# Performance work log

Hardware: AMD Instinct MI355X
Metric: run time of the kernel (lower is better)

The kernel has to match this reference:

```python
import jax, jax.numpy as jnp
import numpy as np
from jax import lax

NH = 8        # num_heads
C = 256       # embedding_dim
WS = 5        # window_size
DN = ('NCHW', 'OIHW', 'NCHW')


def setup_inputs() -> dict:
    key = jax.random.key(0)
    ks = jax.random.split(key, 6)
    B, H, W = 16, 64, 64
    hd = C // NH  # per-head dim = pos_embed_dim
    return {
        "src": jax.random.normal(ks[0], (B, C, H, W), jnp.float32),
        "rel_pos_embed": jax.random.normal(ks[1], (hd, WS, WS), jnp.float32) * 0.02,
        "qkv_w": jax.random.normal(ks[2], (3 * C, C), jnp.float32) * (C ** -0.5),
        "cpe_w": jax.random.normal(ks[3], (C, C, 3, 3), jnp.float32) * (1.0 / np.sqrt(C * 9)),
        "cpe_b": jnp.zeros((C,), jnp.float32),
        "out_w": jax.random.normal(ks[4], (C, C), jnp.float32) * (C ** -0.5),
        "out_b": jnp.zeros((C,), jnp.float32),
    }


def reference(src, rel_pos_embed, qkv_w, cpe_w, cpe_b, out_w, out_b):
    B, Cc, H, W = src.shape
    hd = Cc // NH
    scale = hd ** -0.5

    # conv positional encoding (3x3 conv) + residual
    x = lax.conv_general_dilated(src, cpe_w, (1, 1), [(1, 1), (1, 1)],
                                 dimension_numbers=DN) + cpe_b[None, :, None, None] + src

    # 1x1 qkv conv as a GEMM over channels
    qkv = jnp.einsum('oc,bchw->bohw', qkv_w, x)
    q, k, v = jnp.split(qkv, 3, axis=1)
    q = q.reshape(B * NH, hd, H, W)
    k = k.reshape(B * NH, hd, H, W)
    v = v.reshape(B * NH, hd, H, W)

    # linear (lambda) attention: softmax over spatial positions of k
    kf = jax.nn.softmax(k.reshape(B * NH, hd, H * W), axis=-1)   # (b' i n)
    vf = v.reshape(B * NH, hd, H * W)                            # (b' o n)
    content_lambda = jnp.einsum('bin,bon->bio', kf, vf)          # (b' i o), tiny
    qf = q.reshape(B * NH, hd, H * W) * scale
    content = jnp.einsum('bin,bio->bon', qf, content_lambda).reshape(B * NH, hd, H, W)

    # depthwise conv positional lambda on v
    pad = WS // 2
    pos_lambda = lax.conv_general_dilated(v, rel_pos_embed[:, None], (1, 1),
                                          [(pad, pad), (pad, pad)],
                                          dimension_numbers=DN,
                                          feature_group_count=hd)
    result = (content + q * pos_lambda).reshape(B, Cc, H, W)

    # 1x1 output projection
    return jnp.einsum('oc,bchw->bohw', out_w, result) + out_b[None, :, None, None]
```

## Files before the change

kernel.cpp:

```cpp
#include <hip/hip_runtime.h>


typedef unsigned short u16;
typedef __bf16 bf16x8 __attribute__((ext_vector_type(8)));
typedef float f32x4 __attribute__((ext_vector_type(4)));
#define HW 4096

__device__ __forceinline__ float bf2f(u16 u){
  unsigned v = ((unsigned)u) << 16;
  return __builtin_bit_cast(float, v);
}
__device__ __forceinline__ u16 f2bf(float f){
  unsigned u = __builtin_bit_cast(unsigned, f);
  u = u + 0x7fffu + ((u >> 16) & 1u);
  return (u16)(u >> 16);
}
__device__ __forceinline__ unsigned pack2(float a, float b){
  return (unsigned)f2bf(a) | ((unsigned)f2bf(b) << 16);
}
__device__ __forceinline__ void unpack2(unsigned u, float& a, float& b){
  a = bf2f((u16)(u & 0xffffu)); b = bf2f((u16)(u >> 16));
}
__device__ __forceinline__ void unp8(uint4 r, float* v){
  unpack2(r.x, v[0], v[1]); unpack2(r.y, v[2], v[3]);
  unpack2(r.z, v[4], v[5]); unpack2(r.w, v[6], v[7]);
}
__device__ __forceinline__ int swz(int p){ return (p&3) ^ ((p>>2)&3); }

__device__ __forceinline__ void gl2lds16(const u16* g, u16* l){
  __builtin_amdgcn_global_load_lds((__attribute__((address_space(1))) void*)g,
                                   (__attribute__((address_space(3))) void*)l, 16, 0, 0);
}

__global__ void zero_border(u16* __restrict__ xpad){
  int idx = blockIdx.x*256 + threadIdx.x;
  int g = idx & 31;
  int p = idx >> 5;
  int b = p / 260; int r = p - b*260;
  int y, x;
  if (r < 66)      { y = 0;      x = r; }
  else if (r < 132){ y = 65;     x = r-66; }
  else if (r < 196){ y = r-131;  x = 0; }
  else             { y = r-195;  x = 65; }
  *(uint4*)&xpad[((size_t)b*4356 + (size_t)y*66 + x)*256 + g*8] = uint4{0,0,0,0};
}

__global__ __launch_bounds__(256) void to_nhwc(const float* __restrict__ src,
                                               u16* __restrict__ xpad){
  __shared__ u16 sl[64*264];
  const int t = threadIdx.x, w = t>>6, lane = t&63;
  const int y = blockIdx.x, b = blockIdx.y;
  for (int cc = 0; cc < 64; ++cc){
    const int c = cc*4 + w;
    float v = src[((size_t)(b*256 + c))*HW + y*64 + lane];
    sl[lane*264 + c] = f2bf(v);
  }
  __syncthreads();
  #pragma unroll
  for (int i = 0; i < 8; ++i){
    int idx = t + 256*i;
    int p = idx >> 5, g = idx & 31;
    uint4 v = *(const uint4*)&sl[p*264 + g*8];
    *(uint4*)&xpad[((size_t)b*4356 + (size_t)(y+1)*66 + (p+1))*256 + g*8] = v;
  }
}

__global__ void repack_w(const float* __restrict__ cpe_w, const float* __restrict__ qkv_w,
                         const float* __restrict__ out_w, u16* __restrict__ wrb,
                         u16* __restrict__ wq, u16* __restrict__ wo){
  int idx = blockIdx.x*256 + threadIdx.x;
  if (idx < 589824){
    int kk = idx >> 16, o = (idx >> 8) & 255, c = idx & 255;
    wrb[idx] = f2bf(cpe_w[((o*256 + c)*9) + kk]);
  } else if (idx < 786432){
    int j = idx - 589824;
    wq[j] = f2bf(qkv_w[j]);
  } else {
    int j = idx - 786432;
    wo[j] = f2bf(out_w[j]);
  }
}

__global__ __launch_bounds__(256) void conv_mfma(const u16* __restrict__ xpad,
    const u16* __restrict__ wrb, const float* __restrict__ bias,
    u16* __restrict__ xout){
  __shared__ u16 As[4096];
  __shared__ u16 Bs[4096];
  const int t = threadIdx.x, w = t>>6, lane = t&63;
  const int idx = blockIdx.x;
  const int x8 = idx&7, q = idx>>3;
  const int ot = q & 1, nb = (q>>1)*8 + x8;
  const int pg = nb*128;
  const int b = pg>>12, hw0 = pg&4095, y0 = hw0>>6;
  const int o0 = ot*128;
  const size_t xb = (size_t)b*4356;
  const int sp = t>>2;
  const int cs = (t&3) ^ swz(sp);
  const u16* agp0 = xpad + (xb + (size_t)(y0+1)*66 + sp + 1)*256 + cs*8;
  const u16* agp1 = agp0 + 66*256;
  const u16* bgp0 = wrb + (size_t)(o0 + sp)*256 + cs*8;
  const u16* bgp1 = bgp0 + 64*256;
  const int wm = w&1, wn = w>>1;
  int a_off[4], b_off[4];
  #pragma unroll
  for (int i = 0; i < 4; ++i){
    int p = wm*64 + i*16 + (lane&15);
    a_off[i] = p*32 + ((((lane>>4) ^ swz(p)) & 3) << 3);
    int r = wn*64 + i*16 + (lane&15);
    b_off[i] = r*32 + ((((lane>>4) ^ swz(r)) & 3) << 3);
  }
  f32x4 acc[4][4];
  #pragma unroll
  for (int i=0;i<4;++i)
    #pragma unroll
    for (int j=0;j<4;++j) acc[i][j] = f32x4{0.f,0.f,0.f,0.f};

  for (int c0 = 0; c0 < 256; c0 += 32){
    for (int kk = 0; kk < 9; ++kk){
      const int toff = ((kk/3 - 1)*66 + (kk%3 - 1))*256;
      __syncthreads();
      gl2lds16(agp0 + toff + c0, &As[t*8]);
      gl2lds16(agp1 + toff + c0, &As[2048 + t*8]);
      gl2lds16(bgp0 + kk*65536 + c0, &Bs[t*8]);
      gl2lds16(bgp1 + kk*65536 + c0, &Bs[2048 + t*8]);
      __syncthreads();
      bf16x8 af[4], bfr[4];
      #pragma unroll
      for (int i = 0; i < 4; ++i){
        af[i]  = __builtin_bit_cast(bf16x8, *(const uint4*)&As[a_off[i]]);
        bfr[i] = __builtin_bit_cast(bf16x8, *(const uint4*)&Bs[b_off[i]]);
      }
      #pragma unroll
      for (int mt = 0; mt < 4; ++mt)
        #pragma unroll
        for (int nt = 0; nt < 4; ++nt)
          acc[mt][nt] = __builtin_amdgcn_mfma_f32_16x16x32_bf16(bfr[nt], af[mt], acc[mt][nt], 0,0,0);
    }
  }
  #pragma unroll
  for (int nt = 0; nt < 4; ++nt){
    const int och4 = o0 + wn*64 + nt*16 + (lane>>4)*4;
    float4 b4 = *(const float4*)&bias[och4];
    #pragma unroll
    for (int mt = 0; mt < 4; ++mt){
      const int px = wm*64 + mt*16 + (lane&15);
      const int hw = hw0 + px;
      const int y = hw>>6, x = hw&63;
      ushort4 r4 = *(const ushort4*)&xpad[(xb + (size_t)(y+1)*66 + x + 1)*256 + och4];
      ushort4 s;
      s.x = f2bf(acc[mt][nt][0] + b4.x + bf2f(r4.x));
      s.y = f2bf(acc[mt][nt][1] + b4.y + bf2f(r4.y));
      s.z = f2bf(acc[mt][nt][2] + b4.z + bf2f(r4.z));
      s.w = f2bf(acc[mt][nt][3] + b4.w + bf2f(r4.w));
      *(ushort4*)&xout[(size_t)(pg + px)*256 + och4] = s;
    }
  }
}

template<int NO, int NOT, bool F32OUT>
__global__ __launch_bounds__(256) void gemm_mfma(const u16* __restrict__ act,
    const u16* __restrict__ wt, const float* __restrict__ bias, void* __restrict__ out){
  __shared__ u16 As[4096];
  __shared__ u16 Bs[4096];
  const int t = threadIdx.x, w = t>>6, lane = t&63;
  const int idx = blockIdx.x;
  const int x8 = idx&7, q = idx>>3;
  const int ot = q % NOT, nb = (q / NOT)*8 + x8;
  const int pg = nb*128, o0 = ot*128;
  const int sp = t>>2;
  const int cs = (t&3) ^ swz(sp);
  const u16* agp0 = act + (size_t)(pg + sp)*256 + cs*8;
  const u16* agp1 = agp0 + 64*256;
  const u16* bgp0 = wt + (size_t)(o0 + sp)*256 + cs*8;
  const u16* bgp1 = bgp0 + 64*256;
  const int wm = w&1, wn = w>>1;
  int a_off[4], b_off[4];
  #pragma unroll
  for (int i = 0; i < 4; ++i){
    int p = wm*64 + i*16 + (lane&15);
    a_off[i] = p*32 + ((((lane>>4) ^ swz(p)) & 3) << 3);
    int r = wn*64 + i*16 + (lane&15);
    b_off[i] = r*32 + ((((lane>>4) ^ swz(r)) & 3) << 3);
  }
  f32x4 acc[4][4];
  #pragma unroll
  for (int i=0;i<4;++i)
    #pragma unroll
    for (int j=0;j<4;++j) acc[i][j] = f32x4{0.f,0.f,0.f,0.f};

  for (int c0 = 0; c0 < 256; c0 += 32){
    __syncthreads();
    gl2lds16(agp0 + c0, &As[t*8]);
    gl2lds16(agp1 + c0, &As[2048 + t*8]);
    gl2lds16(bgp0 + c0, &Bs[t*8]);
    gl2lds16(bgp1 + c0, &Bs[2048 + t*8]);
    __syncthreads();
    bf16x8 af[4], bfr[4];
    #pragma unroll
    for (int i = 0; i < 4; ++i){
      af[i]  = __builtin_bit_cast(bf16x8, *(const uint4*)&As[a_off[i]]);
      bfr[i] = __builtin_bit_cast(bf16x8, *(const uint4*)&Bs[b_off[i]]);
    }
    #pragma unroll
    for (int mt = 0; mt < 4; ++mt)
      #pragma unroll
      for (int nt = 0; nt < 4; ++nt){
        if constexpr (F32OUT)
          acc[mt][nt] = __builtin_amdgcn_mfma_f32_16x16x32_bf16(af[mt], bfr[nt], acc[mt][nt], 0,0,0);
        else
          acc[mt][nt] = __builtin_amdgcn_mfma_f32_16x16x32_bf16(bfr[nt], af[mt], acc[mt][nt], 0,0,0);
      }
  }
  if constexpr (F32OUT){
    const int col = lane&15, row_l = (lane>>4)*4;
    const int b = pg>>12, hw0 = pg&4095;
    float* op = (float*)out;
    #pragma unroll
    for (int nt = 0; nt < 4; ++nt){
      const int och = o0 + wn*64 + nt*16 + col;
      const float bo = bias[och];
      #pragma unroll
      for (int mt = 0; mt < 4; ++mt){
        const int pl = wm*64 + mt*16 + row_l;
        float4 v;
        v.x = acc[mt][nt][0]+bo; v.y = acc[mt][nt][1]+bo;
        v.z = acc[mt][nt][2]+bo; v.w = acc[mt][nt][3]+bo;
        *(float4*)&op[((size_t)b*256 + och)*HW + hw0 + pl] = v;
      }
    }
  } else {
    u16* op = (u16*)out;
    #pragma unroll
    for (int nt = 0; nt < 4; ++nt){
      const int och4 = o0 + wn*64 + nt*16 + (lane>>4)*4;
      #pragma unroll
      for (int mt = 0; mt < 4; ++mt){
        const int px = wm*64 + mt*16 + (lane&15);
        ushort4 s;
        s.x = f2bf(acc[mt][nt][0]); s.y = f2bf(acc[mt][nt][1]);
        s.z = f2bf(acc[mt][nt][2]); s.w = f2bf(acc[mt][nt][3]);
        *(ushort4*)&op[(size_t)(pg + px)*NO + och4] = s;
      }
    }
  }
}

__global__ void zero_cl(float* __restrict__ cl){
  cl[blockIdx.x*256 + threadIdx.x] = 0.f;
}

__global__ __launch_bounds__(64) void lambda_kern(const u16* __restrict__ qkv,
                                                  float* __restrict__ cl,
                                                  float* __restrict__ S){
  __shared__ float Kl[64*36];
  __shared__ float Vl[64*36];
  const int t = threadIdx.x;
  const int bp = blockIdx.x, split = blockIdx.y;
  const int b = bp>>3, h = bp&7;
  const int ig = t&7, og = t>>3;
  float acc[4][4];
  float sacc[4] = {0.f,0.f,0.f,0.f};
  #pragma unroll
  for (int i=0;i<4;++i)
    #pragma unroll
    for (int j=0;j<4;++j) acc[i][j] = 0.f;
  for (int chunk = 0; chunk < 8; ++chunk){
    const int n = split*512 + chunk*64 + t;
    const u16* kp = qkv + (size_t)(b*HW + n)*768 + 256 + h*32;
    const u16* vp = kp + 256;
    uint4 k4[4], v4[4];
    #pragma unroll
    for (int qq=0;qq<4;++qq){ k4[qq] = ((const uint4*)kp)[qq]; v4[qq] = ((const uint4*)vp)[qq]; }
    __syncthreads();
    #pragma unroll
    for (int qq=0;qq<4;++qq){
      float kv[8], vv[8]; unp8(k4[qq], kv); unp8(v4[qq], vv);
      #pragma unroll
      for (int e=0;e<8;++e) kv[e] = __expf(kv[e]);
      *(float4*)&Kl[t*36 + qq*8]     = float4{kv[0],kv[1],kv[2],kv[3]};
      *(float4*)&Kl[t*36 + qq*8 + 4] = float4{kv[4],kv[5],kv[6],kv[7]};
      *(float4*)&Vl[t*36 + qq*8]     = float4{vv[0],vv[1],vv[2],vv[3]};
      *(float4*)&Vl[t*36 + qq*8 + 4] = float4{vv[4],vv[5],vv[6],vv[7]};
    }
    __syncthreads();
    for (int p = 0; p < 64; ++p){
      float4 kf = *(const float4*)&Kl[p*36 + ig*4];
      float4 vf = *(const float4*)&Vl[p*36 + og*4];
      float kfa[4] = {kf.x,kf.y,kf.z,kf.w};
      float vfa[4] = {vf.x,vf.y,vf.z,vf.w};
      #pragma unroll
      for (int i=0;i<4;++i){
        sacc[i] += kfa[i];
        #pragma unroll
        for (int j=0;j<4;++j) acc[i][j] = fmaf(kfa[i], vfa[j], acc[i][j]);
      }
    }
  }
  #pragma unroll
  for (int i=0;i<4;++i)
    #pragma unroll
    for (int j=0;j<4;++j)
      atomicAdd(&cl[(size_t)bp*1024 + (ig*4+i)*32 + og*4+j], acc[i][j]);
  if (og == 0){
    #pragma unroll
    for (int i=0;i<4;++i) atomicAdd(&S[bp*32 + ig*4 + i], sacc[i]);
  }
}

__global__ __launch_bounds__(256) void content_combine(const u16* __restrict__ qkv,
    const float* __restrict__ cl, const float* __restrict__ S,
    const float* __restrict__ rel, u16* __restrict__ res){
  __shared__ u16 vt[12800];
  __shared__ float cls[1024];
  __shared__ float relT[800];
  const int t = threadIdx.x;
  const int tile = blockIdx.x, h = blockIdx.y, b = blockIdx.z;
  const int x0 = (tile&3)*16, y0 = (tile>>2)*16;
  for (int idx = t; idx < 1024; idx += 256){
    const float sinv = 0.17677669529663687f / S[(b*8+h)*32 + (idx>>5)];
    cls[idx] = cl[(size_t)(b*8+h)*1024 + idx] * sinv;
  }
  for (int idx = t; idx < 800; idx += 256){
    int tap = idx>>5, ch = idx&31;
    relT[idx] = rel[ch*25 + tap];
  }
  #pragma unroll
  for (int i = 0; i < 7; ++i){
    int idx = t + 256*i;
    if (idx < 1600){
      int hp = idx>>2, g = idx&3;
      int hy = hp/20, hx = hp - hy*20;
      int y = y0 + hy - 2, x = x0 + hx - 2;
      uint4 v = uint4{0,0,0,0};
      if ((unsigned)y < 64u && (unsigned)x < 64u)
        v = *(const uint4*)&qkv[(size_t)(b*HW + y*64 + x)*768 + 512 + h*32 + g*8];
      *(uint4*)&vt[hp*32 + ((g ^ (hx&3))<<3)] = v;
    }
  }
  __syncthreads();
  const int py = t>>4, px = t&15;
  const int pix = b*HW + (y0+py)*64 + x0 + px;
  const u16* qp = qkv + (size_t)pix*768 + h*32;
  float qv[32];
  {
    uint4 q0 = ((const uint4*)qp)[0], q1 = ((const uint4*)qp)[1];
    uint4 q2 = ((const uint4*)qp)[2], q3 = ((const uint4*)qp)[3];
    unp8(q0, qv); unp8(q1, qv+8); unp8(q2, qv+16); unp8(q3, qv+24);
  }
  float outv[32];
  #pragma unroll
  for (int j=0;j<32;++j) outv[j] = 0.f;
  for (int i = 0; i < 32; ++i){
    const float qi = qv[i];
    #pragma unroll
    for (int g = 0; g < 8; ++g){
      float4 c4 = *(const float4*)&cls[i*32 + g*4];
      outv[g*4+0] = fmaf(qi, c4.x, outv[g*4+0]);
      outv[g*4+1] = fmaf(qi, c4.y, outv[g*4+1]);
      outv[g*4+2] = fmaf(qi, c4.z, outv[g*4+2]);
      outv[g*4+3] = fmaf(qi, c4.w, outv[g*4+3]);
    }
  }
  #pragma unroll
  for (int chg = 0; chg < 4; ++chg){
    float pos[8];
    #pragma unroll
    for (int j=0;j<8;++j) pos[j] = 0.f;
    #pragma unroll
    for (int dy = 0; dy < 5; ++dy)
      #pragma unroll
      for (int dx = 0; dx < 5; ++dx){
        int hx = px + dx;
        uint4 v4 = *(const uint4*)&vt[((py+dy)*20 + hx)*32 + ((chg ^ (hx&3))<<3)];
        float vv[8]; unp8(v4, vv);
        float4 r0 = *(const float4*)&relT[(dy*5+dx)*32 + chg*8];
        float4 r1 = *(const float4*)&relT[(dy*5+dx)*32 + chg*8 + 4];
        pos[0]=fmaf(r0.x, vv[0], pos[0]); pos[1]=fmaf(r0.y, vv[1], pos[1]);
        pos[2]=fmaf(r0.z, vv[2], pos[2]); pos[3]=fmaf(r0.w, vv[3], pos[3]);
        pos[4]=fmaf(r1.x, vv[4], pos[4]); pos[5]=fmaf(r1.y, vv[5], pos[5]);
        pos[6]=fmaf(r1.z, vv[6], pos[6]); pos[7]=fmaf(r1.w, vv[7], pos[7]);
      }
    #pragma unroll
    for (int j=0;j<8;++j) outv[chg*8+j] = fmaf(qv[chg*8+j], pos[j], outv[chg*8+j]);
  }
  u16* rp = res + (size_t)pix*256 + h*32;
  #pragma unroll
  for (int g = 0; g < 4; ++g){
    uint4 o_;
    o_.x = pack2(outv[g*8+0], outv[g*8+1]);
    o_.y = pack2(outv[g*8+2], outv[g*8+3]);
    o_.z = pack2(outv[g*8+4], outv[g*8+5]);
    o_.w = pack2(outv[g*8+6], outv[g*8+7]);
    ((uint4*)rp)[g] = o_;
  }
}

extern "C" void kernel_launch(void* const* d_in, const int* in_sizes, int n_in,
                              void* d_out, int out_size, void* d_ws, size_t ws_size,
                              hipStream_t stream) {
  const float* src   = (const float*)d_in[0];
  const float* rel   = (const float*)d_in[1];
  const float* qkv_w = (const float*)d_in[2];
  const float* cpe_w = (const float*)d_in[3];
  const float* cpe_b = (const float*)d_in[4];
  const float* out_w = (const float*)d_in[5];
  const float* out_b = (const float*)d_in[6];
  char* ws = (char*)d_ws;
  u16*   qkv  = (u16*)(ws);
  u16*   xpad = (u16*)(ws);
  u16*   xbuf = (u16*)(ws + 100663296);
  float* cl   = (float*)(ws + 134217728);
  float* S    = (float*)(ws + 134742016);
  u16*   wrb  = (u16*)(ws + 134758400);
  u16*   wq   = (u16*)(ws + 135938048);
  u16*   wo   = (u16*)(ws + 136331264);

  zero_border<<<dim3(520), dim3(256), 0, stream>>>(xpad);
  to_nhwc<<<dim3(64, 16), dim3(256), 0, stream>>>(src, xpad);
  repack_w<<<dim3(3328), dim3(256), 0, stream>>>(cpe_w, qkv_w, out_w, wrb, wq, wo);
  conv_mfma<<<dim3(1024), dim3(256), 0, stream>>>(xpad, wrb, cpe_b, xbuf);
  gemm_mfma<768,6,false><<<dim3(3072), dim3(256), 0, stream>>>(xbuf, wq, nullptr, (void*)qkv);
  zero_cl<<<dim3(528), dim3(256), 0, stream>>>(cl);
  lambda_kern<<<dim3(128, 8), dim3(64), 0, stream>>>(qkv, cl, S);
  content_combine<<<dim3(16, 8, 16), dim3(256), 0, stream>>>(qkv, cl, S, rel, xbuf);
  gemm_mfma<256,2,true><<<dim3(1024), dim3(256), 0, stream>>>(xbuf, wo, out_b, d_out);
}
```

Baseline: 468.1 us.

## Use MFMA for content lambda product and split lambda reduction finer

The content_combine kernel now computes the q·lambda product with bf16 MFMA instructions. The lambda matrix is stored transposed in bf16 in swizzled shared memory, and each wave handles four rows of 16 pixels. The positional depthwise conv is remapped so each lane produces 8 output channels matching the MFMA output layout, with a new vt swizzle. lambda_kern doubles its split count so each block covers half as many pixels, which adds parallelism at the cost of more atomics. Lambda is rounded to bf16, which adds some precision loss.

```diff
diff --git a/kernel.cpp b/kernel.cpp
--- a/kernel.cpp
+++ b/kernel.cpp
@@ -264,8 +264,8 @@
   for (int i=0;i<4;++i)
     #pragma unroll
     for (int j=0;j<4;++j) acc[i][j] = 0.f;
-  for (int chunk = 0; chunk < 8; ++chunk){
-    const int n = split*512 + chunk*64 + t;
+  for (int chunk = 0; chunk < 4; ++chunk){
+    const int n = split*256 + chunk*64 + t;
     const u16* kp = qkv + (size_t)(b*HW + n)*768 + 256 + h*32;
     const u16* vp = kp + 256;
     uint4 k4[4], v4[4];
@@ -311,14 +311,19 @@
     const float* __restrict__ cl, const float* __restrict__ S,
     const float* __restrict__ rel, u16* __restrict__ res){
   __shared__ u16 vt[12800];
-  __shared__ float cls[1024];
+  __shared__ u16 clsT[1024];
   __shared__ float relT[800];
   const int t = threadIdx.x;
   const int tile = blockIdx.x, h = blockIdx.y, b = blockIdx.z;
   const int x0 = (tile&3)*16, y0 = (tile>>2)*16;
-  for (int idx = t; idx < 1024; idx += 256){
-    const float sinv = 0.17677669529663687f / S[(b*8+h)*32 + (idx>>5)];
-    cls[idx] = cl[(size_t)(b*8+h)*1024 + idx] * sinv;
+  const int bp = b*8 + h;
+  const float scale = 0.17677669529663687f;
+  #pragma unroll
+  for (int it = 0; it < 4; ++it){
+    int idx = t + 256*it;
+    int och = idx & 31, i = idx >> 5;
+    float val = cl[(size_t)bp*1024 + i*32 + och] * (scale / S[bp*32 + i]);
+    clsT[och*32 + (((i>>3) ^ (och&3))<<3) + (i&7)] = f2bf(val);
   }
   for (int idx = t; idx < 800; idx += 256){
     int tap = idx>>5, ch = idx&31;
@@ -328,70 +333,68 @@
   for (int i = 0; i < 7; ++i){
     int idx = t + 256*i;
     if (idx < 1600){
-      int hp = idx>>2, g = idx&3;
+      int hp = idx>>2, gg = idx&3;
       int hy = hp/20, hx = hp - hy*20;
       int y = y0 + hy - 2, x = x0 + hx - 2;
       uint4 v = uint4{0,0,0,0};
       if ((unsigned)y < 64u && (unsigned)x < 64u)
-        v = *(const uint4*)&qkv[(size_t)(b*HW + y*64 + x)*768 + 512 + h*32 + g*8];
-      *(uint4*)&vt[hp*32 + ((g ^ (hx&3))<<3)] = v;
+        v = *(const uint4*)&qkv[(size_t)(b*HW + y*64 + x)*768 + 512 + h*32 + gg*8];
+      *(uint4*)&vt[hp*32 + (((gg*2) ^ (hp&6))<<2)] = v;
     }
   }
   __syncthreads();
-  const int py = t>>4, px = t&15;
-  const int pix = b*HW + (y0+py)*64 + x0 + px;
-  const u16* qp = qkv + (size_t)pix*768 + h*32;
-  float qv[32];
-  {
-    uint4 q0 = ((const uint4*)qp)[0], q1 = ((const uint4*)qp)[1];
-    uint4 q2 = ((const uint4*)qp)[2], q3 = ((const uint4*)qp)[3];
-    unp8(q0, qv); unp8(q1, qv+8); unp8(q2, qv+16); unp8(q3, qv+24);
-  }
-  float outv[32];
-  #pragma unroll
-  for (int j=0;j<32;++j) outv[j] = 0.f;
-  for (int i = 0; i < 32; ++i){
-    const float qi = qv[i];
-    #pragma unroll
-    for (int g = 0; g < 8; ++g){
-      float4 c4 = *(const float4*)&cls[i*32 + g*4];
-      outv[g*4+0] = fmaf(qi, c4.x, outv[g*4+0]);
-      outv[g*4+1] = fmaf(qi, c4.y, outv[g*4+1]);
-      outv[g*4+2] = fmaf(qi, c4.z, outv[g*4+2]);
-      outv[g*4+3] = fmaf(qi, c4.w, outv[g*4+3]);
-    }
-  }
-  #pragma unroll
-  for (int chg = 0; chg < 4; ++chg){
-    float pos[8];
-    #pragma unroll
-    for (int j=0;j<8;++j) pos[j] = 0.f;
-    #pragma unroll
-    for (int dy = 0; dy < 5; ++dy)
+
+  const int w = t>>6, lane = t&63;
+  const int m15 = lane&15, q4 = lane>>4;
+  bf16x8 af0 = __builtin_bit_cast(bf16x8, *(const uint4*)&clsT[m15*32 + ((q4 ^ (m15&3))<<3)]);
+  bf16x8 af1 = __builtin_bit_cast(bf16x8, *(const uint4*)&clsT[(16+m15)*32 + ((q4 ^ ((16+m15)&3))<<3)]);
+  f32x4 ca[4], cb[4];
+  #pragma unroll
+  for (int j = 0; j < 4; ++j){
+    const int py = w*4 + j;
+    const int pix = b*HW + (y0+py)*64 + x0 + m15;
+    bf16x8 bq = __builtin_bit_cast(bf16x8,
+        *(const uint4*)&qkv[(size_t)pix*768 + h*32 + q4*8]);
+    ca[j] = __builtin_amdgcn_mfma_f32_16x16x32_bf16(af0, bq, f32x4{0.f,0.f,0.f,0.f}, 0,0,0);
+    cb[j] = __builtin_amdgcn_mfma_f32_16x16x32_bf16(af1, bq, f32x4{0.f,0.f,0.f,0.f}, 0,0,0);
+  }
+  const int och4a = q4*4;
+  #pragma unroll
+  for (int j = 0; j < 4; ++j){
+    const int py = w*4 + j;
+    const int pix = b*HW + (y0+py)*64 + x0 + m15;
+    float pa[4] = {0.f,0.f,0.f,0.f}, pb[4] = {0.f,0.f,0.f,0.f};
+    #pragma unroll
+    for (int dy = 0; dy < 5; ++dy){
+      const int rowb = (py+dy)*20 + m15;
       #pragma unroll
       for (int dx = 0; dx < 5; ++dx){
-        int hx = px + dx;
-        uint4 v4 = *(const uint4*)&vt[((py+dy)*20 + hx)*32 + ((chg ^ (hx&3))<<3)];
-        float vv[8]; unp8(v4, vv);
-        float4 r0 = *(const float4*)&relT[(dy*5+dx)*32 + chg*8];
-        float4 r1 = *(const float4*)&relT[(dy*5+dx)*32 + chg*8 + 4];
-        pos[0]=fmaf(r0.x, vv[0], pos[0]); pos[1]=fmaf(r0.y, vv[1], pos[1]);
-        pos[2]=fmaf(r0.z, vv[2], pos[2]); pos[3]=fmaf(r0.w, vv[3], pos[3]);
-        pos[4]=fmaf(r1.x, vv[4], pos[4]); pos[5]=fmaf(r1.y, vv[5], pos[5]);
-        pos[6]=fmaf(r1.z, vv[6], pos[6]); pos[7]=fmaf(r1.w, vv[7], pos[7]);
-      }
-    #pragma unroll
-    for (int j=0;j<8;++j) outv[chg*8+j] = fmaf(qv[chg*8+j], pos[j], outv[chg*8+j]);
-  }
-  u16* rp = res + (size_t)pix*256 + h*32;
-  #pragma unroll
-  for (int g = 0; g < 4; ++g){
-    uint4 o_;
-    o_.x = pack2(outv[g*8+0], outv[g*8+1]);
-    o_.y = pack2(outv[g*8+2], outv[g*8+3]);
-    o_.z = pack2(outv[g*8+4], outv[g*8+5]);
-    o_.w = pack2(outv[g*8+6], outv[g*8+7]);
-    ((uint4*)rp)[g] = o_;
+        const int hp = rowb + dx, m = hp&6;
+        ushort4 va = *(const ushort4*)&vt[hp*32 + ((q4 ^ m)<<2)];
+        ushort4 vb = *(const ushort4*)&vt[hp*32 + (((q4+4) ^ m)<<2)];
+        float4 ra = *(const float4*)&relT[(dy*5+dx)*32 + och4a];
+        float4 rb = *(const float4*)&relT[(dy*5+dx)*32 + och4a + 16];
+        pa[0] = fmaf(ra.x, bf2f(va.x), pa[0]); pa[1] = fmaf(ra.y, bf2f(va.y), pa[1]);
+        pa[2] = fmaf(ra.z, bf2f(va.z), pa[2]); pa[3] = fmaf(ra.w, bf2f(va.w), pa[3]);
+        pb[0] = fmaf(rb.x, bf2f(vb.x), pb[0]); pb[1] = fmaf(rb.y, bf2f(vb.y), pb[1]);
+        pb[2] = fmaf(rb.z, bf2f(vb.z), pb[2]); pb[3] = fmaf(rb.w, bf2f(vb.w), pb[3]);
+      }
+    }
+    const u16* qp = qkv + (size_t)pix*768 + h*32;
+    ushort4 qa = *(const ushort4*)&qp[och4a];
+    ushort4 qb = *(const ushort4*)&qp[och4a + 16];
+    ushort4 sa, sb;
+    sa.x = f2bf(ca[j][0] + bf2f(qa.x)*pa[0]);
+    sa.y = f2bf(ca[j][1] + bf2f(qa.y)*pa[1]);
+    sa.z = f2bf(ca[j][2] + bf2f(qa.z)*pa[2]);
+    sa.w = f2bf(ca[j][3] + bf2f(qa.w)*pa[3]);
+    sb.x = f2bf(cb[j][0] + bf2f(qb.x)*pb[0]);
+    sb.y = f2bf(cb[j][1] + bf2f(qb.y)*pb[1]);
+    sb.z = f2bf(cb[j][2] + bf2f(qb.z)*pb[2]);
+    sb.w = f2bf(cb[j][3] + bf2f(qb.w)*pb[3]);
+    u16* rp = res + (size_t)pix*256 + h*32;
+    *(ushort4*)&rp[och4a]      = sa;
+    *(ushort4*)&rp[och4a + 16] = sb;
   }
 }
 
@@ -421,7 +424,7 @@
   conv_mfma<<<dim3(1024), dim3(256), 0, stream>>>(xpad, wrb, cpe_b, xbuf);
   gemm_mfma<768,6,false><<<dim3(3072), dim3(256), 0, stream>>>(xbuf, wq, nullptr, (void*)qkv);
   zero_cl<<<dim3(528), dim3(256), 0, stream>>>(cl);
-  lambda_kern<<<dim3(128, 8), dim3(64), 0, stream>>>(qkv, cl, S);
+  lambda_kern<<<dim3(128, 16), dim3(64), 0, stream>>>(qkv, cl, S);
   content_combine<<<dim3(16, 8, 16), dim3(256), 0, stream>>>(qkv, cl, S, rel, xbuf);
   gemm_mfma<256,2,true><<<dim3(1024), dim3(256), 0, stream>>>(xbuf, wo, out_b, d_out);
 }
```

Result: slower. 477.8 us (+2.1%).
